# Performance work log

Measured on AMD Instinct MI355X. Metric: run time of the kernel, lower is better.

## Reference

```python
import jax, jax.numpy as jnp
import numpy as np

N_EMBD = 768
BLOCK_SIZE = 2048
ATTN_SPAN = 128
LN_EPS = 1e-5


def _band_mask(T, span):
    # mask[i, j] = 1 iff 0 <= i - j < span  (causal sliding window incl. diagonal)
    i = jnp.arange(T)[:, None]
    j = jnp.arange(T)[None, :]
    d = i - j
    return ((d >= 0) & (d < span)).astype(jnp.float32)


def setup_inputs() -> dict:
    key = jax.random.key(0)
    k1, k2, k3 = jax.random.split(key, 3)
    B, T, D = 8, BLOCK_SIZE, N_EMBD
    x = jax.random.normal(k1, (B, T, D), dtype=jnp.float32)
    W_qkv = jax.random.normal(k2, (D, 3 * D), dtype=jnp.float32) * (1.0 / np.sqrt(D))
    b_qkv = jax.random.normal(k3, (3 * D,), dtype=jnp.float32) * 0.02
    ln_w = jnp.ones((D,), dtype=jnp.float32)
    ln_b = jnp.zeros((D,), dtype=jnp.float32)
    return {"x": x, "W_qkv": W_qkv, "b_qkv": b_qkv, "ln_w": ln_w, "ln_b": ln_b}


def _layer_norm(h, w, b):
    mu = jnp.mean(h, axis=-1, keepdims=True)
    var = jnp.mean(jnp.square(h - mu), axis=-1, keepdims=True)
    return (h - mu) * jax.lax.rsqrt(var + LN_EPS) * w + b


def reference(x, W_qkv, b_qkv, ln_w, ln_b):
    B, T, D = x.shape
    qkv = x @ W_qkv + b_qkv                      # [B, T, 3D]
    q, k, v = jnp.split(qkv, 3, axis=-1)         # each [B, T, D]
    scale = jnp.float32(1.0 / np.sqrt(N_EMBD * ATTN_SPAN))
    scores = jnp.einsum('bid,bjd->bij', q, k) * scale   # [B, T, T]
    mask = _band_mask(T, ATTN_SPAN)              # [T, T]
    scores = scores * mask                       # zero outside sliding window
    out = jnp.einsum('bij,bjd->bid', scores, v)  # [B, T, D]
    return _layer_norm(out, ln_w, ln_b)
```

## Files before the change

kernel.cpp:

```cpp
#include <hip/hip_runtime.h>
#include <cstdint>
#include <cstddef>

typedef __attribute__((ext_vector_type(8))) short bf16x8;
typedef __attribute__((ext_vector_type(4))) float f32x4;
typedef __attribute__((ext_vector_type(8))) unsigned short u16x8;

#define NB 8
#define NT 2048
#define ND 768
#define NC 2304
#define NM (NB*NT)
#define SPAN 128

__device__ __forceinline__ unsigned short f2bf(float f) {
    unsigned int u = __builtin_bit_cast(unsigned int, f);
    u += 0x7fffu + ((u >> 16) & 1u);
    return (unsigned short)(u >> 16);
}

#define GLOAD16(G, L) __builtin_amdgcn_global_load_lds( \
    (const __attribute__((address_space(1))) unsigned int*)(G), \
    (__attribute__((address_space(3))) unsigned int*)(L), 16, 0, 0)

__global__ void k_conv_x(const float* __restrict__ x, unsigned short* __restrict__ xb) {
    int i = blockIdx.x * 256 + threadIdx.x;
    const float4* p = (const float4*)x + (size_t)i * 2;
    float4 a = p[0], b = p[1];
    u16x8 v;
    v[0] = f2bf(a.x); v[1] = f2bf(a.y); v[2] = f2bf(a.z); v[3] = f2bf(a.w);
    v[4] = f2bf(b.x); v[5] = f2bf(b.y); v[6] = f2bf(b.z); v[7] = f2bf(b.w);
    *((u16x8*)xb + i) = v;
}

__global__ void k_conv_wT(const float* __restrict__ W, unsigned short* __restrict__ wT) {
    __shared__ unsigned short tile[64][72];
    const int k0 = blockIdx.x * 64, n0 = blockIdx.y * 64;
    const int tid = threadIdx.x;
    for (int e = 0; e < 16; ++e) {
        int idx = e * 256 + tid;
        int r = idx >> 6, c = idx & 63;
        tile[r][c] = f2bf(W[(size_t)(k0 + r) * NC + n0 + c]);
    }
    __syncthreads();
    for (int e = 0; e < 16; ++e) {
        int idx = e * 256 + tid;
        int r = idx & 63, c = idx >> 6;
        wT[(size_t)(n0 + c) * ND + k0 + r] = tile[r][c];
    }
}

__global__ void k_gemm(const unsigned short* __restrict__ xb,
                       const unsigned short* __restrict__ wT,
                       const float* __restrict__ bq,
                       unsigned short* __restrict__ qb,
                       unsigned short* __restrict__ kb,
                       unsigned short* __restrict__ vb) {
    __shared__ unsigned short Asw[128 * 64];
    __shared__ unsigned short Bsw[128 * 64];
    const int tid = threadIdx.x;
    const int lane = tid & 63, w = tid >> 6;
    const int m0 = blockIdx.x * 128, n0 = blockIdx.y * 128;
    const int wr = (w >> 1) * 64, wc = (w & 1) * 64;

    f32x4 acc[4][4];
    const f32x4 zf = {0.f, 0.f, 0.f, 0.f};
#pragma unroll
    for (int i = 0; i < 4; ++i)
#pragma unroll
        for (int j = 0; j < 4; ++j) acc[i][j] = zf;

    for (int kc = 0; kc < 12; ++kc) {
        if (kc) __syncthreads();
#pragma unroll
        for (int t = 0; t < 4; ++t) {
            int chunk = w * 4 + t;
            int p = chunk * 1024 + lane * 16;
            int row = p >> 7;
            int col = (p & 127) ^ ((row & 7) << 4);
            GLOAD16(xb + (size_t)(m0 + row) * ND + kc * 64 + (col >> 1), Asw + chunk * 512);
            GLOAD16(wT + (size_t)(n0 + row) * ND + kc * 64 + (col >> 1), Bsw + chunk * 512);
        }
        __syncthreads();
#pragma unroll
        for (int kk = 0; kk < 2; ++kk) {
            bf16x8 af[4], bg[4];
#pragma unroll
            for (int i = 0; i < 4; ++i) {
                int r = wr + i * 16 + (lane & 15);
                af[i] = *(const bf16x8*)((const char*)Asw + r * 128 +
                        ((kk * 64 + (lane >> 4) * 16) ^ ((r & 7) << 4)));
                int c = wc + i * 16 + (lane & 15);
                bg[i] = *(const bf16x8*)((const char*)Bsw + c * 128 +
                        ((kk * 64 + (lane >> 4) * 16) ^ ((c & 7) << 4)));
            }
#pragma unroll
            for (int i = 0; i < 4; ++i)
#pragma unroll
                for (int j = 0; j < 4; ++j)
                    acc[i][j] = __builtin_amdgcn_mfma_f32_16x16x32_bf16(af[i], bg[j], acc[i][j], 0, 0, 0);
        }
    }

    const int third = n0 / ND;
    unsigned short* ob = third == 0 ? qb : (third == 1 ? kb : vb);
    const int nl0 = n0 - third * ND + wc;
#pragma unroll
    for (int j = 0; j < 4; ++j) {
        int nl = nl0 + j * 16 + (lane & 15);
        float bias = bq[third * ND + nl];
#pragma unroll
        for (int i = 0; i < 4; ++i) {
#pragma unroll
            for (int r = 0; r < 4; ++r) {
                int m = m0 + wr + i * 16 + (lane >> 4) * 4 + r;
                ob[(size_t)m * ND + nl] = f2bf(acc[i][j][r] + bias);
            }
        }
    }
}

__global__ void k_transpose_v(const unsigned short* __restrict__ vb, unsigned short* __restrict__ vT) {
    __shared__ unsigned short tile[64][72];
    const int t0 = blockIdx.x * 64, d0 = blockIdx.y * 64, b = blockIdx.z;
    const int tid = threadIdx.x;
#pragma unroll
    for (int e = 0; e < 2; ++e) {
        int vi = e * 256 + tid;
        int r = vi >> 3, c8 = vi & 7;
        u16x8 v = *(const u16x8*)(vb + ((size_t)b * NT + t0 + r) * ND + d0 + c8 * 8);
        *(u16x8*)(&tile[r][c8 * 8]) = v;
    }
    __syncthreads();
#pragma unroll
    for (int e = 0; e < 2; ++e) {
        int vi = e * 256 + tid;
        int dr = vi >> 3, t8 = vi & 7;
        u16x8 v;
#pragma unroll
        for (int q = 0; q < 8; ++q) v[q] = tile[t8 * 8 + q][dr];
        *(u16x8*)(vT + ((size_t)b * ND + d0 + dr) * NT + t0 + t8 * 8) = v;
    }
}

__global__ __launch_bounds__(1024) void k_attn(const unsigned short* __restrict__ qb,
                       const unsigned short* __restrict__ kb,
                       const unsigned short* __restrict__ vT,
                       const float* __restrict__ lnw,
                       const float* __restrict__ lnb,
                       float* __restrict__ out) {
    __shared__ char smem[123904];
    unsigned short* S = (unsigned short*)smem;
    char* R = smem + 25600;

    const int tid = threadIdx.x, lane = tid & 63, w = tid >> 6;
    const int bid = blockIdx.x;
    const int nid = (bid & 7) * 32 + (bid >> 3);
    const int b = nid >> 5;
    const int q0 = (nid & 31) * 64;
    const size_t rowQ = (size_t)b * NT + q0;
    const size_t rowK = (size_t)b * NT;
    const size_t vbase = (size_t)b * ND * NT;

    f32x4 sacc[3];
    const f32x4 zf = {0.f, 0.f, 0.f, 0.f};
#pragma unroll
    for (int s = 0; s < 3; ++s) sacc[s] = zf;

    const int qrow = (w >> 2) * 16 + (lane & 15);
    const int kct = (w & 3) * 3;

    auto stage_qk = [&](int dc, int cur) {
        char* L = R + cur * 32768;
#pragma unroll
        for (int e = 0; e < 2; ++e) {
            int s = w * 128 + e * 64 + lane;
            const unsigned short* src;
            if (s < 512) {
                int r = s >> 3, sl = s & 7;
                src = qb + (rowQ + r) * ND + dc * 64 + 8 * (sl ^ (r & 7));
            } else {
                int t = s - 512;
                int r = t >> 3, sl = t & 7;
                int j = q0 - 128 + r; if (j < 0) j = 0;
                src = kb + (rowK + j) * ND + dc * 64 + 8 * (sl ^ (r & 7));
            }
            GLOAD16(src, L + (w * 128 + e * 64) * 16);
        }
    };

    stage_qk(0, 0);
    __syncthreads();
    for (int dc = 0; dc < 12; ++dc) {
        int cur = dc & 1;
        if (dc < 11) stage_qk(dc + 1, cur ^ 1);
        const char* Lq = R + cur * 32768;
        const char* Lk = Lq + 8192;
#pragma unroll
        for (int kk = 0; kk < 2; ++kk) {
            int bq_ = (((lane >> 4) * 16 + kk * 64)) ^ ((qrow & 7) << 4);
            bf16x8 aq = *(const bf16x8*)(Lq + qrow * 128 + bq_);
#pragma unroll
            for (int s = 0; s < 3; ++s) {
                int krow = (kct + s) * 16 + (lane & 15);
                int bk_ = (((lane >> 4) * 16 + kk * 64)) ^ ((krow & 7) << 4);
                bf16x8 bk = *(const bf16x8*)(Lk + krow * 128 + bk_);
                sacc[s] = __builtin_amdgcn_mfma_f32_16x16x32_bf16(aq, bk, sacc[s], 0, 0, 0);
            }
        }
        __syncthreads();
    }

    const float scl = 0.0031894436f;
#pragma unroll
    for (int s = 0; s < 3; ++s) {
        int jl = (kct + s) * 16 + (lane & 15);
        int j = q0 - 128 + jl;
#pragma unroll
        for (int e = 0; e < 4; ++e) {
            int il = (w >> 2) * 16 + (lane >> 4) * 4 + e;
            int d = (q0 + il) - j;
            float v = (d >= 0 && d < SPAN && j >= 0) ? sacc[s][e] * scl : 0.0f;
            S[il * 200 + jl] = f2bf(v);
        }
    }

    auto stage_v = [&](int c, int cur) {
        char* L = R + cur * 49152;
        int j0 = q0 - 128 + c * 32;
#pragma unroll
        for (int e = 0; e < 3; ++e) {
            int s = w * 192 + e * 64 + lane;
            int d = s >> 2, sl = s & 3;
            int j = j0 + 8 * (sl ^ (d & 3)); if (j < 0) j = 0;
            GLOAD16(vT + vbase + (size_t)d * NT + j, L + (w * 192 + e * 64) * 16);
        }
    };

    f32x4 acc[4][3];
#pragma unroll
    for (int rt = 0; rt < 4; ++rt)
#pragma unroll
        for (int ct = 0; ct < 3; ++ct) acc[rt][ct] = zf;

    stage_v(0, 0);
    __syncthreads();
    for (int c = 0; c < 6; ++c) {
        int cur = c & 1;
        if (c < 5) stage_v(c + 1, cur ^ 1);
        const char* Lv = R + cur * 49152;
        bf16x8 as[4], bv[3];
#pragma unroll
        for (int rt = 0; rt < 4; ++rt)
            as[rt] = *(const bf16x8*)((const char*)S + (rt * 16 + (lane & 15)) * 400 + c * 64 + (lane >> 4) * 16);
#pragma unroll
        for (int ct = 0; ct < 3; ++ct) {
            int d = (w * 3 + ct) * 16 + (lane & 15);
            bv[ct] = *(const bf16x8*)(Lv + d * 64 + (((lane >> 4) * 16) ^ ((d & 3) << 4)));
        }
#pragma unroll
        for (int rt = 0; rt < 4; ++rt)
#pragma unroll
            for (int ct = 0; ct < 3; ++ct)
                acc[rt][ct] = __builtin_amdgcn_mfma_f32_16x16x32_bf16(as[rt], bv[ct], acc[rt][ct], 0, 0, 0);
        __syncthreads();
    }

    float psum[4][4], pssq[4][4];
#pragma unroll
    for (int rt = 0; rt < 4; ++rt)
#pragma unroll
        for (int e = 0; e < 4; ++e) {
            float s = 0.f, q = 0.f;
#pragma unroll
            for (int ct = 0; ct < 3; ++ct) { float v = acc[rt][ct][e]; s += v; q += v * v; }
            psum[rt][e] = s; pssq[rt][e] = q;
        }
#pragma unroll
    for (int mx = 1; mx < 16; mx <<= 1)
#pragma unroll
        for (int rt = 0; rt < 4; ++rt)
#pragma unroll
            for (int e = 0; e < 4; ++e) {
                psum[rt][e] += __shfl_xor(psum[rt][e], mx, 64);
                pssq[rt][e] += __shfl_xor(pssq[rt][e], mx, 64);
            }

    float* P = (float*)R;
    float* F = (float*)(R + 8192);
    if ((lane & 15) == 0) {
#pragma unroll
        for (int rt = 0; rt < 4; ++rt)
#pragma unroll
            for (int e = 0; e < 4; ++e) {
                int r = rt * 16 + (lane >> 4) * 4 + e;
                P[(r * 16 + w) * 2] = psum[rt][e];
                P[(r * 16 + w) * 2 + 1] = pssq[rt][e];
            }
    }
    __syncthreads();
    if (tid < 64) {
        float s = 0.f, q = 0.f;
#pragma unroll
        for (int ww = 0; ww < 16; ++ww) { s += P[(tid * 16 + ww) * 2]; q += P[(tid * 16 + ww) * 2 + 1]; }
        float mu = s * (1.0f / 768.0f);
        float var = q * (1.0f / 768.0f) - mu * mu;
        F[tid * 2] = mu;
        F[tid * 2 + 1] = rsqrtf(var + 1e-5f);
    }
    __syncthreads();

    float lw[3], lb_[3];
#pragma unroll
    for (int ct = 0; ct < 3; ++ct) {
        int dcol = (w * 3 + ct) * 16 + (lane & 15);
        lw[ct] = lnw[dcol]; lb_[ct] = lnb[dcol];
    }
#pragma unroll
    for (int rt = 0; rt < 4; ++rt)
#pragma unroll
        for (int e = 0; e < 4; ++e) {
            int row = rt * 16 + (lane >> 4) * 4 + e;
            float mu = F[row * 2], rs = F[row * 2 + 1];
            float* rowp = out + (rowQ + row) * ND;
#pragma unroll
            for (int ct = 0; ct < 3; ++ct) {
                int dcol = (w * 3 + ct) * 16 + (lane & 15);
                rowp[dcol] = (acc[rt][ct][e] - mu) * rs * lw[ct] + lb_[ct];
            }
        }
}

extern "C" void kernel_launch(void* const* d_in, const int* in_sizes, int n_in,
                              void* d_out, int out_size, void* d_ws, size_t ws_size,
                              hipStream_t stream) {
    const float* x   = (const float*)d_in[0];
    const float* W   = (const float*)d_in[1];
    const float* bqv = (const float*)d_in[2];
    const float* lnw = (const float*)d_in[3];
    const float* lnb = (const float*)d_in[4];
    float* out = (float*)d_out;

    char* ws = (char*)d_ws;
    const size_t SZ_XB = (size_t)NM * ND * 2;
    const size_t SZ_WT = (size_t)NC * ND * 2;
    const size_t SZ_P  = (size_t)NM * ND * 2;
    unsigned short* xb = (unsigned short*)ws;
    unsigned short* wT = (unsigned short*)(ws + SZ_XB);
    unsigned short* qb = (unsigned short*)(ws + SZ_XB + SZ_WT);
    unsigned short* kb = (unsigned short*)(ws + SZ_XB + SZ_WT + SZ_P);
    unsigned short* vb = (unsigned short*)(ws + SZ_XB + SZ_WT + 2 * SZ_P);
    unsigned short* vT = xb;

    k_conv_x<<<dim3(NM * ND / (256 * 8)), dim3(256), 0, stream>>>(x, xb);
    k_conv_wT<<<dim3(ND / 64, NC / 64), dim3(256), 0, stream>>>(W, wT);
    k_gemm<<<dim3(NM / 128, NC / 128), dim3(256), 0, stream>>>(xb, wT, bqv, qb, kb, vb);
    k_transpose_v<<<dim3(NT / 64, ND / 64, NB), dim3(256), 0, stream>>>(vb, vT);
    k_attn<<<dim3(256), dim3(1024), 0, stream>>>(qb, kb, vT, lnw, lnb, out);
}
```

Before: 127.8 us.

## Rewrite QKV GEMM with 256x256 double-buffered tiles and fused V transpose

Replaces the 128x128 single-buffered QKV GEMM with a 256x256 tile, 512-thread kernel that double-buffers A/B tiles in 128KB LDS. Global-to-LDS loads are interleaved with MFMA phases using explicit waitcnt, barriers and setprio. The V output is transposed through LDS in the GEMM epilogue, so the separate transpose kernel and its extra pass over V are gone. The cost is higher register and LDS pressure, only 576 blocks, and fragile hand-tuned synchronisation.

```diff
diff --git a/kernel.cpp b/kernel.cpp
--- a/kernel.cpp
+++ b/kernel.cpp
@@ -5,6 +5,7 @@
 typedef __attribute__((ext_vector_type(8))) short bf16x8;
 typedef __attribute__((ext_vector_type(4))) float f32x4;
 typedef __attribute__((ext_vector_type(8))) unsigned short u16x8;
+typedef __attribute__((ext_vector_type(4))) unsigned short u16x4;
 
 #define NB 8
 #define NT 2048
@@ -50,96 +51,190 @@
     }
 }
 
-__global__ void k_gemm(const unsigned short* __restrict__ xb,
+__global__ __launch_bounds__(512, 2) void k_gemm(const unsigned short* __restrict__ xb,
                        const unsigned short* __restrict__ wT,
                        const float* __restrict__ bq,
                        unsigned short* __restrict__ qb,
                        unsigned short* __restrict__ kb,
-                       unsigned short* __restrict__ vb) {
-    __shared__ unsigned short Asw[128 * 64];
-    __shared__ unsigned short Bsw[128 * 64];
-    const int tid = threadIdx.x;
-    const int lane = tid & 63, w = tid >> 6;
-    const int m0 = blockIdx.x * 128, n0 = blockIdx.y * 128;
-    const int wr = (w >> 1) * 64, wc = (w & 1) * 64;
-
-    f32x4 acc[4][4];
+                       unsigned short* __restrict__ vT) {
+    __shared__ char lds[131072];
+    const int tid = threadIdx.x, lane = tid & 63, w = tid >> 6;
+    const int bid = blockIdx.x;
+    const int mb = (bid & 7) * 8 + ((bid >> 3) & 7);
+    const int nb = bid >> 6;
+    const int m0 = mb * 256, n0 = nb * 256;
+    const int wr = (w >> 2) * 128, wc = (w & 3) * 64;
+
+    auto stageA = [&](int t, int h) {
+        char* dst = lds + (t & 1) * 32768 + h * 16384 + w * 2048;
+        const unsigned short* sb = xb + (size_t)(m0 + h * 128) * ND + t * 64;
+#pragma unroll
+        for (int e = 0; e < 2; ++e) {
+            int s = w * 128 + e * 64 + lane;
+            int r = s >> 3, sl = s & 7;
+            GLOAD16(sb + (size_t)r * ND + 8 * (sl ^ (r & 7)), dst + e * 1024);
+        }
+    };
+    auto stageB = [&](int t, int h) {
+        char* dst = lds + 65536 + (t & 1) * 32768 + h * 16384 + w * 2048;
+        const unsigned short* sb = wT + (size_t)(n0 + h * 128) * ND + t * 64;
+#pragma unroll
+        for (int e = 0; e < 2; ++e) {
+            int s = w * 128 + e * 64 + lane;
+            int r = s >> 3, sl = s & 7;
+            GLOAD16(sb + (size_t)r * ND + 8 * (sl ^ (r & 7)), dst + e * 1024);
+        }
+    };
+
+    f32x4 acc[2][4][4];
     const f32x4 zf = {0.f, 0.f, 0.f, 0.f};
 #pragma unroll
-    for (int i = 0; i < 4; ++i)
-#pragma unroll
-        for (int j = 0; j < 4; ++j) acc[i][j] = zf;
-
-    for (int kc = 0; kc < 12; ++kc) {
-        if (kc) __syncthreads();
-#pragma unroll
-        for (int t = 0; t < 4; ++t) {
-            int chunk = w * 4 + t;
-            int p = chunk * 1024 + lane * 16;
-            int row = p >> 7;
-            int col = (p & 127) ^ ((row & 7) << 4);
-            GLOAD16(xb + (size_t)(m0 + row) * ND + kc * 64 + (col >> 1), Asw + chunk * 512);
-            GLOAD16(wT + (size_t)(n0 + row) * ND + kc * 64 + (col >> 1), Bsw + chunk * 512);
-        }
-        __syncthreads();
-#pragma unroll
-        for (int kk = 0; kk < 2; ++kk) {
-            bf16x8 af[4], bg[4];
-#pragma unroll
-            for (int i = 0; i < 4; ++i) {
-                int r = wr + i * 16 + (lane & 15);
-                af[i] = *(const bf16x8*)((const char*)Asw + r * 128 +
-                        ((kk * 64 + (lane >> 4) * 16) ^ ((r & 7) << 4)));
-                int c = wc + i * 16 + (lane & 15);
-                bg[i] = *(const bf16x8*)((const char*)Bsw + c * 128 +
-                        ((kk * 64 + (lane >> 4) * 16) ^ ((c & 7) << 4)));
-            }
-#pragma unroll
-            for (int i = 0; i < 4; ++i)
-#pragma unroll
-                for (int j = 0; j < 4; ++j)
-                    acc[i][j] = __builtin_amdgcn_mfma_f32_16x16x32_bf16(af[i], bg[j], acc[i][j], 0, 0, 0);
-        }
-    }
-
-    const int third = n0 / ND;
-    unsigned short* ob = third == 0 ? qb : (third == 1 ? kb : vb);
-    const int nl0 = n0 - third * ND + wc;
-#pragma unroll
-    for (int j = 0; j < 4; ++j) {
-        int nl = nl0 + j * 16 + (lane & 15);
-        float bias = bq[third * ND + nl];
-#pragma unroll
-        for (int i = 0; i < 4; ++i) {
-#pragma unroll
-            for (int r = 0; r < 4; ++r) {
-                int m = m0 + wr + i * 16 + (lane >> 4) * 4 + r;
-                ob[(size_t)m * ND + nl] = f2bf(acc[i][j][r] + bias);
-            }
-        }
-    }
-}
-
-__global__ void k_transpose_v(const unsigned short* __restrict__ vb, unsigned short* __restrict__ vT) {
-    __shared__ unsigned short tile[64][72];
-    const int t0 = blockIdx.x * 64, d0 = blockIdx.y * 64, b = blockIdx.z;
-    const int tid = threadIdx.x;
-#pragma unroll
-    for (int e = 0; e < 2; ++e) {
-        int vi = e * 256 + tid;
-        int r = vi >> 3, c8 = vi & 7;
-        u16x8 v = *(const u16x8*)(vb + ((size_t)b * NT + t0 + r) * ND + d0 + c8 * 8);
-        *(u16x8*)(&tile[r][c8 * 8]) = v;
-    }
-    __syncthreads();
-#pragma unroll
-    for (int e = 0; e < 2; ++e) {
-        int vi = e * 256 + tid;
-        int dr = vi >> 3, t8 = vi & 7;
-        u16x8 v;
-#pragma unroll
-        for (int q = 0; q < 8; ++q) v[q] = tile[t8 * 8 + q][dr];
-        *(u16x8*)(vT + ((size_t)b * ND + d0 + dr) * NT + t0 + t8 * 8) = v;
+    for (int s = 0; s < 2; ++s)
+#pragma unroll
+        for (int mi = 0; mi < 4; ++mi)
+#pragma unroll
+            for (int ni = 0; ni < 4; ++ni) acc[s][mi][ni] = zf;
+
+    const int rA = wr + (lane & 15);
+    const int rB = wc + (lane & 15);
+    const int g16 = (lane >> 4) * 16;
+    const int swA = (rA & 7) << 4, swB = (rB & 7) << 4;
+
+    stageB(0, 0); stageB(0, 1); stageA(0, 0); stageA(0, 1);
+    stageB(1, 0); stageB(1, 1);
+    asm volatile("s_waitcnt vmcnt(4)" ::: "memory");
+    __builtin_amdgcn_s_barrier();
+
+#pragma unroll 1
+    for (int q = 0; q < 12; ++q) {
+        const char* Ab = lds + (q & 1) * 32768;
+        const char* Bb = lds + 65536 + (q & 1) * 32768;
+        bf16x8 Af[4], Ag[4], Bf0[4], Bf1[4];
+
+        if (q + 1 < 12) stageA(q + 1, 0);
+#pragma unroll
+        for (int mi = 0; mi < 4; ++mi)
+            Af[mi] = *(const bf16x8*)(Ab + (size_t)(rA + mi * 16) * 128 + (g16 ^ swA));
+#pragma unroll
+        for (int ni = 0; ni < 4; ++ni)
+            Bf0[ni] = *(const bf16x8*)(Bb + (size_t)(rB + ni * 16) * 128 + (g16 ^ swB));
+        __builtin_amdgcn_s_barrier();
+        asm volatile("s_waitcnt lgkmcnt(0)" ::: "memory");
+        __builtin_amdgcn_sched_barrier(0);
+        __builtin_amdgcn_s_setprio(1);
+#pragma unroll
+        for (int mi = 0; mi < 4; ++mi)
+#pragma unroll
+            for (int ni = 0; ni < 4; ++ni)
+                acc[0][mi][ni] = __builtin_amdgcn_mfma_f32_16x16x32_bf16(Af[mi], Bf0[ni], acc[0][mi][ni], 0, 0, 0);
+        __builtin_amdgcn_s_setprio(0);
+        __builtin_amdgcn_s_barrier();
+
+        if (q + 1 < 12) stageA(q + 1, 1);
+#pragma unroll
+        for (int mi = 0; mi < 4; ++mi)
+            Ag[mi] = *(const bf16x8*)(Ab + (size_t)(rA + 64 + mi * 16) * 128 + (g16 ^ swA));
+#pragma unroll
+        for (int ni = 0; ni < 4; ++ni)
+            Bf1[ni] = *(const bf16x8*)(Bb + (size_t)(rB + ni * 16) * 128 + ((64 + g16) ^ swB));
+        __builtin_amdgcn_s_barrier();
+        asm volatile("s_waitcnt lgkmcnt(0)" ::: "memory");
+        __builtin_amdgcn_sched_barrier(0);
+        __builtin_amdgcn_s_setprio(1);
+#pragma unroll
+        for (int mi = 0; mi < 4; ++mi)
+#pragma unroll
+            for (int ni = 0; ni < 4; ++ni)
+                acc[1][mi][ni] = __builtin_amdgcn_mfma_f32_16x16x32_bf16(Ag[mi], Bf0[ni], acc[1][mi][ni], 0, 0, 0);
+        __builtin_amdgcn_s_setprio(0);
+        __builtin_amdgcn_s_barrier();
+
+        if (q + 2 < 12) stageB(q + 2, 0);
+#pragma unroll
+        for (int mi = 0; mi < 4; ++mi)
+            Af[mi] = *(const bf16x8*)(Ab + (size_t)(rA + mi * 16) * 128 + ((64 + g16) ^ swA));
+        __builtin_amdgcn_s_barrier();
+        asm volatile("s_waitcnt lgkmcnt(0)" ::: "memory");
+        __builtin_amdgcn_sched_barrier(0);
+        __builtin_amdgcn_s_setprio(1);
+#pragma unroll
+        for (int mi = 0; mi < 4; ++mi)
+#pragma unroll
+            for (int ni = 0; ni < 4; ++ni)
+                acc[0][mi][ni] = __builtin_amdgcn_mfma_f32_16x16x32_bf16(Af[mi], Bf1[ni], acc[0][mi][ni], 0, 0, 0);
+        __builtin_amdgcn_s_setprio(0);
+        __builtin_amdgcn_s_barrier();
+
+        if (q + 2 < 12) stageB(q + 2, 1);
+#pragma unroll
+        for (int mi = 0; mi < 4; ++mi)
+            Ag[mi] = *(const bf16x8*)(Ab + (size_t)(rA + 64 + mi * 16) * 128 + ((64 + g16) ^ swA));
+        __builtin_amdgcn_s_barrier();
+        asm volatile("s_waitcnt lgkmcnt(0)" ::: "memory");
+        __builtin_amdgcn_sched_barrier(0);
+        __builtin_amdgcn_s_setprio(1);
+#pragma unroll
+        for (int mi = 0; mi < 4; ++mi)
+#pragma unroll
+            for (int ni = 0; ni < 4; ++ni)
+                acc[1][mi][ni] = __builtin_amdgcn_mfma_f32_16x16x32_bf16(Ag[mi], Bf1[ni], acc[1][mi][ni], 0, 0, 0);
+        __builtin_amdgcn_s_setprio(0);
+        if (q < 10) { asm volatile("s_waitcnt vmcnt(4)" ::: "memory"); }
+        else if (q == 10) { asm volatile("s_waitcnt vmcnt(0)" ::: "memory"); }
+        __builtin_amdgcn_s_barrier();
+    }
+
+    const int third = nb / 3;
+    const int nl0 = (nb % 3) * 256 + wc;
+    if (third < 2) {
+        unsigned short* ob = third == 0 ? qb : kb;
+        float bias[4];
+#pragma unroll
+        for (int ni = 0; ni < 4; ++ni) bias[ni] = bq[third * ND + nl0 + ni * 16 + (lane & 15)];
+#pragma unroll
+        for (int s = 0; s < 2; ++s)
+#pragma unroll
+            for (int mi = 0; mi < 4; ++mi)
+#pragma unroll
+                for (int e = 0; e < 4; ++e) {
+                    int m = m0 + wr + (s * 4 + mi) * 16 + (lane >> 4) * 4 + e;
+#pragma unroll
+                    for (int ni = 0; ni < 4; ++ni)
+                        ob[(size_t)m * ND + nl0 + ni * 16 + (lane & 15)] = f2bf(acc[s][mi][ni][e] + bias[ni]);
+                }
+    } else {
+        const int bb = m0 >> 11, t0g = m0 & 2047;
+        unsigned short* vTb = vT + ((size_t)bb * ND + (nb - 6) * 256) * NT;
+        float bias[4];
+#pragma unroll
+        for (int ni = 0; ni < 4; ++ni) bias[ni] = bq[2 * ND + (nb - 6) * 256 + wc + ni * 16 + (lane & 15)];
+        unsigned short* T = (unsigned short*)lds;
+        for (int c = 0; c < 4; ++c) {
+            __builtin_amdgcn_s_barrier();
+            if ((w & 3) == c) {
+#pragma unroll
+                for (int s = 0; s < 2; ++s)
+#pragma unroll
+                    for (int mi = 0; mi < 4; ++mi)
+#pragma unroll
+                        for (int ni = 0; ni < 4; ++ni) {
+                            int d_loc = ni * 16 + (lane & 15);
+                            int t_loc = wr + (s * 4 + mi) * 16 + (lane >> 4) * 4;
+                            u16x4 pk;
+#pragma unroll
+                            for (int e = 0; e < 4; ++e) pk[e] = f2bf(acc[s][mi][ni][e] + bias[ni]);
+                            *(u16x4*)(T + d_loc * 264 + t_loc) = pk;
+                        }
+            }
+            __builtin_amdgcn_s_barrier();
+#pragma unroll
+            for (int e2 = 0; e2 < 4; ++e2) {
+                int slot = e2 * 512 + tid;
+                int dd = slot >> 5, tc = (slot & 31) * 8;
+                u16x8 v = *(const u16x8*)(T + dd * 264 + tc);
+                *(u16x8*)(vTb + (size_t)(c * 64 + dd) * NT + t0g + tc) = v;
+            }
+        }
     }
 }
 
@@ -349,12 +444,10 @@
     unsigned short* wT = (unsigned short*)(ws + SZ_XB);
     unsigned short* qb = (unsigned short*)(ws + SZ_XB + SZ_WT);
     unsigned short* kb = (unsigned short*)(ws + SZ_XB + SZ_WT + SZ_P);
-    unsigned short* vb = (unsigned short*)(ws + SZ_XB + SZ_WT + 2 * SZ_P);
-    unsigned short* vT = xb;
+    unsigned short* vT = (unsigned short*)(ws + SZ_XB + SZ_WT + 2 * SZ_P);
 
     k_conv_x<<<dim3(NM * ND / (256 * 8)), dim3(256), 0, stream>>>(x, xb);
     k_conv_wT<<<dim3(ND / 64, NC / 64), dim3(256), 0, stream>>>(W, wT);
-    k_gemm<<<dim3(NM / 128, NC / 128), dim3(256), 0, stream>>>(xb, wT, bqv, qb, kb, vb);
-    k_transpose_v<<<dim3(NT / 64, ND / 64, NB), dim3(256), 0, stream>>>(vb, vT);
+    k_gemm<<<dim3(576), dim3(512), 0, stream>>>(xb, wT, bqv, qb, kb, vT);
     k_attn<<<dim3(256), dim3(1024), 0, stream>>>(qb, kb, vT, lnw, lnb, out);
 }
```

After: 130.0 us. No clear change (+1.7%).
